# Optimization experiments

Measured on AMD Instinct MI355X. Metric: run time of the kernel, lower is better.

The kernel has to match this reference:

```python
import jax, jax.numpy as jnp
import numpy as np

B, T, E, H = 4, 2048, 1024, 16
HD = E // H  # head_size = 64


def setup_inputs() -> dict:
    key = jax.random.key(0)
    ks = jax.random.split(key, 6)
    s = 1.0 / np.sqrt(E)
    x = jax.random.normal(ks[0], (B, T, E), dtype=jnp.float32)
    # per-head Q/K/V projection weights, stacked over heads: [H, E, HD]
    Wq = jax.random.uniform(ks[1], (H, E, HD), minval=-s, maxval=s, dtype=jnp.float32)
    Wk = jax.random.uniform(ks[2], (H, E, HD), minval=-s, maxval=s, dtype=jnp.float32)
    Wv = jax.random.uniform(ks[3], (H, E, HD), minval=-s, maxval=s, dtype=jnp.float32)
    Wo = jax.random.uniform(ks[4], (E, E), minval=-s, maxval=s, dtype=jnp.float32)
    bo = jax.random.uniform(ks[5], (E,), minval=-s, maxval=s, dtype=jnp.float32)
    return {"x": x, "Wq": Wq, "Wk": Wk, "Wv": Wv, "Wo": Wo, "bo": bo}


def reference(x, Wq, Wk, Wv, Wo, bo):
    # x: [B,T,E] -> q,k,v: [B,H,T,HD]
    q = jnp.einsum('bte,hed->bhtd', x, Wq)
    k = jnp.einsum('bte,hed->bhtd', x, Wk)
    v = jnp.einsum('bte,hed->bhtd', x, Wv)
    scale = HD ** -0.5
    scores = jnp.einsum('bhtd,bhsd->bhts', q, k) * scale  # [B,H,T,T]
    causal = jnp.tril(jnp.ones((T, T), dtype=bool))
    scores = jnp.where(causal, scores, -jnp.inf)
    wei = jax.nn.softmax(scores, axis=-1)  # dropout is identity in eval
    out = jnp.einsum('bhts,bhsd->bhtd', wei, v)  # [B,H,T,HD]
    out = out.transpose(0, 2, 1, 3).reshape(B, T, E)  # concat heads
    return out @ Wo.T + bo
```

## Files before the change

kernel.cpp:

```cpp
#include <hip/hip_runtime.h>
#include <hip/hip_bf16.h>

#define B_  4
#define T_  2048
#define E_  1024
#define H_  16
#define HD_ 64

typedef __hip_bfloat16 bf16;
typedef unsigned short u16;
using bf16x8 = __attribute__((ext_vector_type(8))) short;
using f32x4  = __attribute__((ext_vector_type(4))) float;

__device__ __forceinline__ float b2f(bf16 x) { return __bfloat162float(x); }
__device__ __forceinline__ bf16  f2b(float x) { return __float2bfloat16(x); }
__device__ __forceinline__ u16 f2b_bits(float x) {
    union { bf16 h; u16 u; } cv; cv.h = __float2bfloat16(x); return cv.u;
}
__device__ __forceinline__ float bits2f(u16 u) {
    union { float f; unsigned int i; } cv; cv.i = ((unsigned int)u) << 16; return cv.f;
}

__device__ __forceinline__ void gld_lds16(const void* g, void* lds) {
    void* gv = (void*)g;
    __builtin_amdgcn_global_load_lds(
        (__attribute__((address_space(1))) void*)gv,
        (__attribute__((address_space(3))) void*)lds, 16, 0, 0);
}

__global__ __launch_bounds__(256) void cast_bf16(
    const float* __restrict__ src, bf16* __restrict__ dst)
{
    size_t i = ((size_t)blockIdx.x * 256 + threadIdx.x) * 8;
    float4 a = *(const float4*)(src + i);
    float4 b = *(const float4*)(src + i + 4);
    u16 o[8] = { f2b_bits(a.x), f2b_bits(a.y), f2b_bits(a.z), f2b_bits(a.w),
                 f2b_bits(b.x), f2b_bits(b.y), f2b_bits(b.z), f2b_bits(b.w) };
    *(uint4*)(dst + i) = *(const uint4*)o;
}

__global__ __launch_bounds__(256) void cast_w_t(
    const float* __restrict__ Wq, const float* __restrict__ Wk,
    const float* __restrict__ Wv, bf16* __restrict__ Wt)
{
    const float* W = (blockIdx.z == 0) ? Wq : (blockIdx.z == 1) ? Wk : Wv;
    const float scl = (blockIdx.z == 0) ? 0.125f : 1.0f;
    bf16* dst = Wt + (size_t)blockIdx.z * (H_ * HD_ * E_);
    const int h = blockIdx.y, k0 = blockIdx.x * 64;
    __shared__ float Ws[64][65];
    const int tid = threadIdx.x;
    {
        int kk = tid >> 2, d0 = (tid & 3) * 16;
        const float* p = W + ((size_t)h * E_ + k0 + kk) * HD_ + d0;
        #pragma unroll
        for (int i = 0; i < 4; i++) {
            float4 f = *(const float4*)(p + i * 4);
            Ws[kk][d0 + i * 4 + 0] = f.x; Ws[kk][d0 + i * 4 + 1] = f.y;
            Ws[kk][d0 + i * 4 + 2] = f.z; Ws[kk][d0 + i * 4 + 3] = f.w;
        }
    }
    __syncthreads();
    {
        int d = tid >> 2, kc = (tid & 3) * 16;
        u16 o[16];
        #pragma unroll
        for (int j = 0; j < 16; j++) o[j] = f2b_bits(Ws[kc + j][d] * scl);
        bf16* p = dst + ((size_t)h * HD_ + d) * E_ + k0 + kc;
        *(uint4*)(p)     = *(const uint4*)&o[0];
        *(uint4*)(p + 8) = *(const uint4*)&o[8];
    }
}

__global__ __launch_bounds__(256) void qkv_mfma(
    const bf16* __restrict__ xb, const bf16* __restrict__ Wt,
    bf16* __restrict__ q, bf16* __restrict__ k, bf16* __restrict__ v)
{
    const int n0 = blockIdx.x * 128;
    const int m0 = blockIdx.y * 128;
    const int z  = n0 >> 10;
    bf16* out = (z == 0) ? q : (z == 1) ? k : v;
    const int tid = threadIdx.x, lane = tid & 63, w = tid >> 6;
    const int wm = w >> 1, wn = w & 1;
    const int quad = lane >> 4, l15 = lane & 15;

    __shared__ __align__(16) u16 smem[2 * 2 * 128 * 64];

    f32x4 acc[4][4];
    #pragma unroll
    for (int i = 0; i < 4; i++)
        #pragma unroll
        for (int j = 0; j < 4; j++) acc[i][j] = f32x4{0.f, 0.f, 0.f, 0.f};

    const int srow = lane >> 3;
    const int scol = ((lane & 7) ^ srow) * 8;
    const bf16* agp = xb + (size_t)(m0 + w * 32 + srow) * E_ + scol;
    const bf16* bgp = Wt + (size_t)(n0 + w * 32 + srow) * E_ + scol;
    const int rsw = l15 & 7;

    #define QSTAGE(b, kk) do {                                                \
        u16* a_ = smem + (b) * 16384 + (w * 32) * 64;                         \
        u16* b_ = smem + (b) * 16384 + 8192 + (w * 32) * 64;                  \
        _Pragma("unroll")                                                     \
        for (int i_ = 0; i_ < 4; i_++) {                                      \
            gld_lds16(agp + (size_t)(i_ * 8) * E_ + (kk), a_ + i_ * 8 * 64);  \
            gld_lds16(bgp + (size_t)(i_ * 8) * E_ + (kk), b_ + i_ * 8 * 64);  \
        }                                                                     \
    } while (0)

    QSTAGE(0, 0);
    int cur = 0;

    for (int k0 = 0; k0 < E_; k0 += 64) {
        if (k0 + 64 < E_) {
            QSTAGE(cur ^ 1, k0 + 64);
            asm volatile("s_waitcnt vmcnt(8)" ::: "memory");
        } else {
            asm volatile("s_waitcnt vmcnt(0)" ::: "memory");
        }
        __builtin_amdgcn_s_barrier();
        __builtin_amdgcn_sched_barrier(0);

        const u16* As = smem + cur * 16384;
        const u16* Bs = As + 8192;
        __builtin_amdgcn_s_setprio(1);
        #pragma unroll
        for (int ks = 0; ks < 2; ks++) {
            const int csw = ((ks * 4 + quad) ^ rsw) * 8;
            bf16x8 af[4];
            #pragma unroll
            for (int i = 0; i < 4; i++)
                af[i] = *(const bf16x8*)&As[(wm * 64 + i * 16 + l15) * 64 + csw];
            #pragma unroll
            for (int j = 0; j < 4; j++) {
                bf16x8 bfr = *(const bf16x8*)&Bs[(wn * 64 + j * 16 + l15) * 64 + csw];
                #pragma unroll
                for (int i = 0; i < 4; i++)
                    acc[i][j] = __builtin_amdgcn_mfma_f32_16x16x32_bf16(af[i], bfr, acc[i][j], 0, 0, 0);
            }
        }
        __builtin_amdgcn_s_setprio(0);

        __builtin_amdgcn_sched_barrier(0);
        __builtin_amdgcn_s_barrier();
        cur ^= 1;
    }
    #undef QSTAGE

    if (z != 2) {
        const int h = ((n0 & 1023) >> 6) + wn;
        #pragma unroll
        for (int i = 0; i < 4; i++)
            #pragma unroll
            for (int r = 0; r < 4; r++) {
                int m = m0 + wm * 64 + i * 16 + quad * 4 + r;
                int bb2 = m >> 11, t = m & (T_ - 1);
                bf16* orow = out + ((size_t)(bb2 * H_ + h) * T_ + t) * HD_;
                #pragma unroll
                for (int j = 0; j < 4; j++)
                    orow[j * 16 + l15] = f2b(acc[i][j][r]);
            }
    } else {
        u16 (*Vt)[136] = (u16(*)[136])smem;
        const int bb2 = m0 >> 11, t0 = m0 & (T_ - 1);
        #pragma unroll
        for (int half = 0; half < 2; half++) {
            __syncthreads();
            if (wn == half) {
                #pragma unroll
                for (int j = 0; j < 4; j++)
                    #pragma unroll
                    for (int i = 0; i < 4; i++) {
                        ushort4 pk;
                        pk.x = f2b_bits(acc[i][j][0]);
                        pk.y = f2b_bits(acc[i][j][1]);
                        pk.z = f2b_bits(acc[i][j][2]);
                        pk.w = f2b_bits(acc[i][j][3]);
                        *(ushort4*)&Vt[j * 16 + l15][wm * 64 + i * 16 + quad * 4] = pk;
                    }
            }
            __syncthreads();
            {
                int dd = tid >> 2, tt = (tid & 3) * 32;
                int h = ((n0 & 1023) >> 6) + half;
                bf16* dst = out + ((size_t)(bb2 * H_ + h) * HD_ + dd) * T_ + t0 + tt;
                #pragma unroll
                for (int u = 0; u < 4; u++)
                    *(uint4*)(dst + u * 8) = *(const uint4*)&Vt[dd][tt + u * 8];
            }
        }
    }
}

__global__ __launch_bounds__(256) void flash_attn(
    const bf16* __restrict__ q, const bf16* __restrict__ k,
    const bf16* __restrict__ vt, bf16* __restrict__ att)
{
    const int bh = blockIdx.x & 63;
    const int qt = 31 - (blockIdx.x >> 6);
    const int q0 = qt * 64;
    const int hh = bh & 15, bb = bh >> 4;
    const int tid = threadIdx.x, lane = tid & 63, wave = tid >> 6;
    const int quad = lane >> 4, l15 = lane & 15;

    __shared__ __align__(16) u16 Ks[2][64 * 64];
    __shared__ __align__(16) u16 Vs[2][64 * 64];
    __shared__ __align__(16) u16 P2[4][1024];

    const size_t baseK = (size_t)bh * T_ * HD_;
    const bf16* vbase = vt + (size_t)bh * (size_t)HD_ * T_;

    const int qg = q0 + wave * 16 + l15;
    const bf16* qrow = q + baseK + (size_t)qg * HD_;
    bf16x8 qfrag[2];
    qfrag[0] = *(const bf16x8*)(qrow + quad * 8);
    qfrag[1] = *(const bf16x8*)(qrow + 32 + quad * 8);

    bf16x8 onesf;
    #pragma unroll
    for (int i = 0; i < 8; i++) onesf[i] = (short)0x3F80;

    f32x4 o[4];
    #pragma unroll
    for (int dt = 0; dt < 4; dt++) o[dt] = f32x4{0.f, 0.f, 0.f, 0.f};
    f32x4 lacc = f32x4{0.f, 0.f, 0.f, 0.f};

    const int q_in = wave * 16 + l15;

    const int srow = lane >> 3;
    const int scol = ((lane & 7) ^ srow) * 8;
    const bf16* kgp = k + baseK + (size_t)(wave * 16 + srow) * HD_ + scol;
    const bf16* vgp = vbase + (size_t)(wave * 16 + srow) * T_ + scol;
    u16* pw = P2[wave];
    const int rsw = l15 & 7;

    #define STAGE(b, s0) do {                                                 \
        gld_lds16(kgp + (size_t)(s0) * HD_,       &Ks[b][wave * 1024]);       \
        gld_lds16(kgp + (size_t)((s0) + 8) * HD_, &Ks[b][wave * 1024 + 512]); \
        gld_lds16(vgp + (s0),                     &Vs[b][wave * 1024]);       \
        gld_lds16(vgp + (s0) + 8 * T_,            &Vs[b][wave * 1024 + 512]); \
    } while (0)

    STAGE(0, 0);
    int cur = 0;

    for (int st = 0; st <= qt; st++) {
        if (st < qt) {
            STAGE(cur ^ 1, (st + 1) * 64);
            asm volatile("s_waitcnt vmcnt(4)" ::: "memory");
        } else {
            asm volatile("s_waitcnt vmcnt(0)" ::: "memory");
        }
        __builtin_amdgcn_s_barrier();
        __builtin_amdgcn_sched_barrier(0);

        f32x4 s[4];
        __builtin_amdgcn_s_setprio(1);
        #pragma unroll
        for (int ct = 0; ct < 4; ct++) {
            f32x4 a = f32x4{0.f, 0.f, 0.f, 0.f};
            #pragma unroll
            for (int ks = 0; ks < 2; ks++) {
                const int csw = ((ks * 4 + quad) ^ rsw) * 8;
                bf16x8 kfrag = *(const bf16x8*)&Ks[cur][(ct * 16 + l15) * 64 + csw];
                a = __builtin_amdgcn_mfma_f32_16x16x32_bf16(kfrag, qfrag[ks], a, 0, 0, 0);
            }
            s[ct] = a;
        }
        __builtin_amdgcn_s_setprio(0);

        if (st == qt) {
            #pragma unroll
            for (int ct = 0; ct < 4; ct++) {
                int sbase = ct * 16 + quad * 4;
                #pragma unroll
                for (int r = 0; r < 4; r++)
                    if (sbase + r > q_in) s[ct][r] = -1e30f;
            }
        }

        #pragma unroll
        for (int ct = 0; ct < 4; ct++) {
            ushort4 pk;
            pk.x = f2b_bits(__builtin_amdgcn_exp2f(__fmaf_rn(s[ct][0], 1.4426950408889634f, -11.541560327111707f)));
            pk.y = f2b_bits(__builtin_amdgcn_exp2f(__fmaf_rn(s[ct][1], 1.4426950408889634f, -11.541560327111707f)));
            pk.z = f2b_bits(__builtin_amdgcn_exp2f(__fmaf_rn(s[ct][2], 1.4426950408889634f, -11.541560327111707f)));
            pk.w = f2b_bits(__builtin_amdgcn_exp2f(__fmaf_rn(s[ct][3], 1.4426950408889634f, -11.541560327111707f)));
            *(ushort4*)&pw[(ct >> 1) * 512
                           + (((((ct & 1) << 1) | (quad >> 1)) * 16 + l15) * 8)
                           + (quad & 1) * 4] = pk;
        }

        __builtin_amdgcn_s_setprio(1);
        #pragma unroll
        for (int ks = 0; ks < 2; ks++) {
            bf16x8 pfrag = *(const bf16x8*)&pw[ks * 512 + (quad * 16 + l15) * 8];
            lacc = __builtin_amdgcn_mfma_f32_16x16x32_bf16(onesf, pfrag, lacc, 0, 0, 0);
            #pragma unroll
            for (int dt = 0; dt < 4; dt++) {
                const int csw = ((ks * 4 + quad) ^ rsw) * 8;
                bf16x8 vfrag = *(const bf16x8*)&Vs[cur][(dt * 16 + l15) * 64 + csw];
                o[dt] = __builtin_amdgcn_mfma_f32_16x16x32_bf16(vfrag, pfrag, o[dt], 0, 0, 0);
            }
        }
        __builtin_amdgcn_s_setprio(0);

        __builtin_amdgcn_sched_barrier(0);
        __builtin_amdgcn_s_barrier();
        cur ^= 1;
    }
    #undef STAGE

    float inv = 1.0f / lacc[0];
    bf16* orow = att + ((size_t)(bb * T_ + qg) * H_ + hh) * HD_;
    #pragma unroll
    for (int dt = 0; dt < 4; dt++) {
        ushort4 pk;
        pk.x = f2b_bits(o[dt][0] * inv);
        pk.y = f2b_bits(o[dt][1] * inv);
        pk.z = f2b_bits(o[dt][2] * inv);
        pk.w = f2b_bits(o[dt][3] * inv);
        *(ushort4*)(orow + dt * 16 + quad * 4) = pk;
    }
}

__global__ __launch_bounds__(256, 3) void out_proj_mfma(
    const bf16* __restrict__ att, const bf16* __restrict__ Wob,
    const float* __restrict__ bo, float* __restrict__ out)
{
    const int m0 = blockIdx.x * 128, n0 = blockIdx.y * 128;
    const int tid = threadIdx.x, lane = tid & 63, w = tid >> 6;
    const int wm = w >> 1, wn = w & 1;
    const int quad = lane >> 4, l15 = lane & 15;

    __shared__ __align__(16) u16 smem[2 * 2 * 128 * 32];

    f32x4 acc[4][4];
    #pragma unroll
    for (int i = 0; i < 4; i++)
        #pragma unroll
        for (int j = 0; j < 4; j++) acc[i][j] = f32x4{0.f, 0.f, 0.f, 0.f};

    const int srow = lane >> 2;
    const int scol = ((lane & 3) ^ (srow & 3)) * 8;
    const bf16* agp = att + (size_t)(m0 + w * 32 + srow) * E_ + scol;
    const bf16* bgp = Wob + (size_t)(n0 + w * 32 + srow) * E_ + scol;
    const int rsw3 = l15 & 3;

    #define OSTAGE(b, kk) do {                                                \
        u16* a_ = smem + (b) * 8192 + (w * 32) * 32;                          \
        u16* b_ = smem + (b) * 8192 + 4096 + (w * 32) * 32;                   \
        _Pragma("unroll")                                                     \
        for (int i_ = 0; i_ < 2; i_++) {                                      \
            gld_lds16(agp + (size_t)(i_ * 16) * E_ + (kk), a_ + i_ * 16 * 32);\
            gld_lds16(bgp + (size_t)(i_ * 16) * E_ + (kk), b_ + i_ * 16 * 32);\
        }                                                                     \
    } while (0)

    OSTAGE(0, 0);
    int cur = 0;

    for (int k0 = 0; k0 < E_; k0 += 32) {
        if (k0 + 32 < E_) {
            OSTAGE(cur ^ 1, k0 + 32);
            asm volatile("s_waitcnt vmcnt(4)" ::: "memory");
        } else {
            asm volatile("s_waitcnt vmcnt(0)" ::: "memory");
        }
        __builtin_amdgcn_s_barrier();
        __builtin_amdgcn_sched_barrier(0);

        const u16* As = smem + cur * 8192;
        const u16* Bs = As + 4096;
        const int csw = (quad ^ rsw3) * 8;
        __builtin_amdgcn_s_setprio(1);
        bf16x8 af[4];
        #pragma unroll
        for (int i = 0; i < 4; i++)
            af[i] = *(const bf16x8*)&As[(wm * 64 + i * 16 + l15) * 32 + csw];
        #pragma unroll
        for (int j = 0; j < 4; j++) {
            bf16x8 bfr = *(const bf16x8*)&Bs[(wn * 64 + j * 16 + l15) * 32 + csw];
            #pragma unroll
            for (int i = 0; i < 4; i++)
                acc[i][j] = __builtin_amdgcn_mfma_f32_16x16x32_bf16(af[i], bfr, acc[i][j], 0, 0, 0);
        }
        __builtin_amdgcn_s_setprio(0);

        __builtin_amdgcn_sched_barrier(0);
        __builtin_amdgcn_s_barrier();
        cur ^= 1;
    }
    #undef OSTAGE

    float bias[4];
    #pragma unroll
    for (int j = 0; j < 4; j++) bias[j] = bo[n0 + wn * 64 + j * 16 + l15];
    #pragma unroll
    for (int i = 0; i < 4; i++)
        #pragma unroll
        for (int r = 0; r < 4; r++) {
            int m = m0 + wm * 64 + i * 16 + quad * 4 + r;
            float* orow = out + (size_t)m * E_ + n0 + wn * 64;
            #pragma unroll
            for (int j = 0; j < 4; j++)
                orow[j * 16 + l15] = acc[i][j][r] + bias[j];
        }
}

extern "C" void kernel_launch(void* const* d_in, const int* in_sizes, int n_in,
                              void* d_out, int out_size, void* d_ws, size_t ws_size,
                              hipStream_t stream)
{
    const float* x  = (const float*)d_in[0];
    const float* Wq = (const float*)d_in[1];
    const float* Wk = (const float*)d_in[2];
    const float* Wv = (const float*)d_in[3];
    const float* Wo = (const float*)d_in[4];
    const float* bo = (const float*)d_in[5];
    float* out = (float*)d_out;

    const size_t elts = (size_t)B_ * H_ * T_ * HD_;
    bf16* att = (bf16*)d_ws;
    bf16* Wt  = att;
    bf16* q   = att + elts;
    bf16* Wob = q;
    bf16* k   = q + elts;
    bf16* v   = k + elts;
    bf16* xb  = (bf16*)d_out;

    cast_bf16<<<dim3((unsigned)(elts / 2048)), 256, 0, stream>>>(x, xb);
    cast_w_t<<<dim3(E_ / 64, H_, 3), 256, 0, stream>>>(Wq, Wk, Wv, Wt);

    qkv_mfma<<<dim3(3 * E_ / 128, (B_ * T_) / 128), 256, 0, stream>>>(xb, Wt, q, k, v);

    flash_attn<<<dim3((T_ / 64) * B_ * H_), 256, 0, stream>>>(q, k, v, att);

    cast_bf16<<<dim3((E_ * E_) / 2048), 256, 0, stream>>>(Wo, Wob);

    out_proj_mfma<<<dim3((B_ * T_) / 128, E_ / 128), 256, 0, stream>>>(att, Wob, bo, out);
}
```

Baseline: 232.7 us.

## Widen attention query tile to 128 with 8 waves and merge input casts

The flash attention kernel now gives each block 128 query rows handled by 8 waves, up from 64 rows and 4 waves. Each K/V tile staged in shared memory is reused by twice as many queries, and each wave issues half as many async loads per tile. Causal masking now uses absolute positions over the last two key tiles. The x cast and the QKV weight cast/transpose are also merged into one launch to save a kernel launch. In exchange, the attention grid has half as many blocks and the larger blocks do more masked work on the diagonal.

```diff
diff --git a/kernel.cpp b/kernel.cpp
--- a/kernel.cpp
+++ b/kernel.cpp
@@ -39,16 +39,28 @@
     *(uint4*)(dst + i) = *(const uint4*)o;
 }
 
-__global__ __launch_bounds__(256) void cast_w_t(
+__global__ __launch_bounds__(256) void cast_all(
+    const float* __restrict__ x,
     const float* __restrict__ Wq, const float* __restrict__ Wk,
-    const float* __restrict__ Wv, bf16* __restrict__ Wt)
-{
-    const float* W = (blockIdx.z == 0) ? Wq : (blockIdx.z == 1) ? Wk : Wv;
-    const float scl = (blockIdx.z == 0) ? 0.125f : 1.0f;
-    bf16* dst = Wt + (size_t)blockIdx.z * (H_ * HD_ * E_);
-    const int h = blockIdx.y, k0 = blockIdx.x * 64;
+    const float* __restrict__ Wv,
+    bf16* __restrict__ xb, bf16* __restrict__ Wt)
+{
+    const int tid = threadIdx.x;
+    if (blockIdx.x < 4096) {
+        size_t i = ((size_t)blockIdx.x * 256 + tid) * 8;
+        float4 a = *(const float4*)(x + i);
+        float4 b = *(const float4*)(x + i + 4);
+        u16 o[8] = { f2b_bits(a.x), f2b_bits(a.y), f2b_bits(a.z), f2b_bits(a.w),
+                     f2b_bits(b.x), f2b_bits(b.y), f2b_bits(b.z), f2b_bits(b.w) };
+        *(uint4*)(xb + i) = *(const uint4*)o;
+        return;
+    }
+    const int wi = blockIdx.x - 4096;
+    const int k0 = (wi & 15) * 64, h = (wi >> 4) & 15, z = wi >> 8;
+    const float* W = (z == 0) ? Wq : (z == 1) ? Wk : Wv;
+    const float scl = (z == 0) ? 0.125f : 1.0f;
+    bf16* dst = Wt + (size_t)z * (H_ * HD_ * E_);
     __shared__ float Ws[64][65];
-    const int tid = threadIdx.x;
     {
         int kk = tid >> 2, d0 = (tid & 3) * 16;
         const float* p = W + ((size_t)h * E_ + k0 + kk) * HD_ + d0;
@@ -191,20 +203,21 @@
     }
 }
 
-__global__ __launch_bounds__(256) void flash_attn(
+__global__ __launch_bounds__(512) void flash_attn(
     const bf16* __restrict__ q, const bf16* __restrict__ k,
     const bf16* __restrict__ vt, bf16* __restrict__ att)
 {
     const int bh = blockIdx.x & 63;
-    const int qt = 31 - (blockIdx.x >> 6);
-    const int q0 = qt * 64;
+    const int qb = 15 - (blockIdx.x >> 6);
+    const int q0 = qb * 128;
+    const int qlast = 2 * qb + 1;
     const int hh = bh & 15, bb = bh >> 4;
     const int tid = threadIdx.x, lane = tid & 63, wave = tid >> 6;
     const int quad = lane >> 4, l15 = lane & 15;
 
     __shared__ __align__(16) u16 Ks[2][64 * 64];
     __shared__ __align__(16) u16 Vs[2][64 * 64];
-    __shared__ __align__(16) u16 P2[4][1024];
+    __shared__ __align__(16) u16 P2[8][1024];
 
     const size_t baseK = (size_t)bh * T_ * HD_;
     const bf16* vbase = vt + (size_t)bh * (size_t)HD_ * T_;
@@ -224,29 +237,26 @@
     for (int dt = 0; dt < 4; dt++) o[dt] = f32x4{0.f, 0.f, 0.f, 0.f};
     f32x4 lacc = f32x4{0.f, 0.f, 0.f, 0.f};
 
-    const int q_in = wave * 16 + l15;
-
     const int srow = lane >> 3;
     const int scol = ((lane & 7) ^ srow) * 8;
-    const bf16* kgp = k + baseK + (size_t)(wave * 16 + srow) * HD_ + scol;
-    const bf16* vgp = vbase + (size_t)(wave * 16 + srow) * T_ + scol;
+    const bf16* kgp = k + baseK + (size_t)(wave * 8 + srow) * HD_ + scol;
+    const bf16* vgp = vbase + (size_t)(wave * 8 + srow) * T_ + scol;
     u16* pw = P2[wave];
     const int rsw = l15 & 7;
 
     #define STAGE(b, s0) do {                                                 \
-        gld_lds16(kgp + (size_t)(s0) * HD_,       &Ks[b][wave * 1024]);       \
-        gld_lds16(kgp + (size_t)((s0) + 8) * HD_, &Ks[b][wave * 1024 + 512]); \
-        gld_lds16(vgp + (s0),                     &Vs[b][wave * 1024]);       \
-        gld_lds16(vgp + (s0) + 8 * T_,            &Vs[b][wave * 1024 + 512]); \
+        gld_lds16(kgp + (size_t)(s0) * HD_, &Ks[b][wave * 512]);              \
+        gld_lds16(vgp + (s0),               &Vs[b][wave * 512]);              \
     } while (0)
 
     STAGE(0, 0);
     int cur = 0;
 
-    for (int st = 0; st <= qt; st++) {
-        if (st < qt) {
+    for (int st = 0; st <= qlast; st++) {
+        const int s0 = st * 64;
+        if (st < qlast) {
             STAGE(cur ^ 1, (st + 1) * 64);
-            asm volatile("s_waitcnt vmcnt(4)" ::: "memory");
+            asm volatile("s_waitcnt vmcnt(2)" ::: "memory");
         } else {
             asm volatile("s_waitcnt vmcnt(0)" ::: "memory");
         }
@@ -268,13 +278,13 @@
         }
         __builtin_amdgcn_s_setprio(0);
 
-        if (st == qt) {
+        if (st >= qlast - 1) {
             #pragma unroll
             for (int ct = 0; ct < 4; ct++) {
-                int sbase = ct * 16 + quad * 4;
+                int sbase = s0 + ct * 16 + quad * 4;
                 #pragma unroll
                 for (int r = 0; r < 4; r++)
-                    if (sbase + r > q_in) s[ct][r] = -1e30f;
+                    if (sbase + r > qg) s[ct][r] = -1e30f;
             }
         }
 
@@ -428,12 +438,11 @@
     bf16* v   = k + elts;
     bf16* xb  = (bf16*)d_out;
 
-    cast_bf16<<<dim3((unsigned)(elts / 2048)), 256, 0, stream>>>(x, xb);
-    cast_w_t<<<dim3(E_ / 64, H_, 3), 256, 0, stream>>>(Wq, Wk, Wv, Wt);
+    cast_all<<<dim3(4096 + 768), 256, 0, stream>>>(x, Wq, Wk, Wv, xb, Wt);
 
     qkv_mfma<<<dim3(3 * E_ / 128, (B_ * T_) / 128), 256, 0, stream>>>(xb, Wt, q, k, v);
 
-    flash_attn<<<dim3((T_ / 64) * B_ * H_), 256, 0, stream>>>(q, k, v, att);
+    flash_attn<<<dim3((T_ / 128) * B_ * H_), 512, 0, stream>>>(q, k, v, att);
 
     cast_bf16<<<dim3((E_ * E_) / 2048), 256, 0, stream>>>(Wo, Wob);
 
```

New measurement: 225.2 us, median of 3. 3.2% less time.
